# Optimization experiments

Measured on AMD Instinct MI355X. Metric: run time of the kernel, lower is better.

## Reference

```python
import jax, jax.numpy as jnp
import numpy as np

THRESHOLD = 0.3

def setup_inputs() -> dict:
    key = jax.random.key(0)
    ks = jax.random.split(key, 8)
    B, T, N, d = 4, 32, 1024, 2
    hd, od, hs, osz = 64, 64, 128, 2
    p = lambda k, sh: jax.random.normal(k, sh, jnp.float32) * 0.1
    return {
        "points": jax.random.uniform(ks[0], (B, T, N, d), jnp.float32),
        "W1": p(ks[1], (hd, d)),   "b1": jnp.zeros((hd,), jnp.float32),
        "W2": p(ks[2], (od, hd)),  "b2": jnp.zeros((od,), jnp.float32),
        "Wg": p(ks[3], (hd, od)),  "bg": jnp.zeros((hd,), jnp.float32),
        "Wih": p(ks[4], (3 * hs, hd)), "Whh": p(ks[5], (3 * hs, hs)),
        "bih": jnp.zeros((3 * hs,), jnp.float32), "bhh": jnp.zeros((3 * hs,), jnp.float32),
        "Wf": p(ks[6], (osz, hs)), "bf": jnp.zeros((osz,), jnp.float32),
    }

def _gcn_step(pts, W1, b1, W2, b2, Wg, bg):
    # pts: [N, d]. Torch detaches node features & adjacency (no grad to points).
    pts = jax.lax.stop_gradient(pts)
    dist = jnp.linalg.norm(pts[:, None, :] - pts[None, :, :], axis=2)  # [N,N]
    A = (dist < THRESHOLD).astype(pts.dtype)
    dinv = 1.0 / jnp.sqrt(A.sum(axis=1))          # rowsum >= 1 (self-loop)
    An = A * dinv[:, None] * dinv[None, :]        # D^{-1/2} A D^{-1/2}
    x = jax.nn.relu((An @ pts) @ W1.T + b1)       # [N, hd]
    x = jax.nn.relu((An @ x) @ W2.T + b2)         # [N, od]
    return x.mean(axis=0) @ Wg.T + bg             # [hd]

def reference(points, W1, b1, W2, b2, Wg, bg, Wih, Whh, bih, bhh, Wf, bf):
    # GCN per (batch, time): [B, T, hd]
    gcn = jax.vmap(jax.vmap(lambda p: _gcn_step(p, W1, b1, W2, b2, Wg, bg)))(points)
    H = Whh.shape[1]

    def gru_step(h, x):  # torch GRU gate order: r, z, n
        gi = x @ Wih.T + bih
        gh = h @ Whh.T + bhh
        ir, iz, inn = jnp.split(gi, 3)
        hr, hz, hn = jnp.split(gh, 3)
        r = jax.nn.sigmoid(ir + hr)
        z = jax.nn.sigmoid(iz + hz)
        n = jnp.tanh(inn + r * hn)
        h_new = (1.0 - z) * n + z * h
        return h_new, h_new

    h0 = jnp.zeros((H,), points.dtype)
    run = lambda xs: jax.lax.scan(gru_step, h0, xs)[1]   # [T, H]
    hs = jax.vmap(run)(gcn)                              # [B, T, H]
    y = hs @ Wf.T + bf                                   # [B, T, out]
    # torch: per-element gru_out.mean(dim=1, keepdim=True) on [1,T,out] -> [1,1,out], stacked -> [B,1,1,out]
    return y.mean(axis=1, keepdims=True)[:, :, None, :]
```

## Files before the change

### kernel.cpp

```cpp
#include <hip/hip_runtime.h>
#include <hip/hip_bf16.h>
#include <math.h>

#define N_PTS 1024
#define BT    128
typedef unsigned int u32;
typedef __attribute__((ext_vector_type(8))) short short8_t;
typedef __attribute__((ext_vector_type(4))) float f32x4;

__device__ __forceinline__ float bfi(u32 bits16) {
    union { u32 u; float f; } v; v.u = bits16 << 16; return v.f;
}
__device__ __forceinline__ unsigned short f2bf(float f) {
    union { float f; u32 u; } v; v.f = f;
    return (unsigned short)((v.u + 0x7FFFu + ((v.u >> 16) & 1u)) >> 16);
}
__device__ __forceinline__ float ldf(const void* p, int i, bool bf) {
    return bf ? bfi(((const unsigned short*)p)[i]) : ((const float*)p)[i];
}
__device__ __forceinline__ float2 ldp(const void* pbase, int j, bool bf) {
    if (bf) {
        u32 w = ((const u32*)pbase)[j];
        return make_float2(bfi(w & 0xFFFFu), bfi(w >> 16));
    }
    return ((const float2*)pbase)[j];
}
__device__ __forceinline__ bool detect_bf16(const void* pts, int tid, int* s_flag) {
    if (tid < 64) {
        u32 w = ((const u32*)pts)[tid];
        float v = bfi(w & 0xFFFFu);
        bool ok = (v >= 0.0f) && (v <= 1.0f);
        unsigned long long m = __ballot(ok);
        if (tid == 0) *s_flag = (m == 0xFFFFFFFFFFFFFFFFull) ? 1 : 0;
    }
    __syncthreads();
    return *s_flag != 0;
}
__device__ __forceinline__ bool is_nb(float px, float py, float qx, float qy) {
    float dx = px - qx, dy = py - qy;
    float d2 = __fadd_rn(__fmul_rn(dx, dx), __fmul_rn(dy, dy));
    return d2 < 0.09f;
}
__device__ __forceinline__ const void* pts_base(const void* pts, int bt, bool bf) {
    return bf ? (const void*)((const unsigned short*)pts + (size_t)bt * N_PTS * 2)
              : (const void*)((const float*)pts + (size_t)bt * N_PTS * 2);
}
__device__ __forceinline__ void gload16(const u32* g, u32* l) {
    __builtin_amdgcn_global_load_lds((const __attribute__((address_space(1))) u32*)g,
                                     (__attribute__((address_space(3))) u32*)l, 16, 0, 0);
}
__device__ __forceinline__ float rdlane(float v, int i) {
    return __int_as_float(__builtin_amdgcn_readlane(__float_as_int(v), i));
}
__device__ __forceinline__ float sigm_f(float x) {
    return __fdividef(1.0f, 1.0f + __expf(-x));
}
__device__ __forceinline__ float tanh_f(float x) {
    float e = __expf(2.0f * x);
    return 1.0f - __fdividef(2.0f, e + 1.0f);
}
__device__ __forceinline__ void build_lut(u32* slut, int tid) {
    if (tid < 16) {
        u32 d0 = ((tid & 1) ? 0x3F80u : 0u) | (((tid & 2) ? 0x3F80u : 0u) << 16);
        u32 d1 = ((tid & 4) ? 0x3F80u : 0u) | (((tid & 8) ? 0x3F80u : 0u) << 16);
        slut[2 * tid] = d0;
        slut[2 * tid + 1] = d1;
    }
}
__device__ __forceinline__ short8_t expand8(const uint2* lut2, u32 by) {
    uint2 lo = lut2[by & 15u], hi = lut2[by >> 4];
    union { uint4 u4; short8_t s8; } cv;
    cv.u4 = make_uint4(lo.x, lo.y, hi.x, hi.y);
    return cv.s8;
}

__global__ __launch_bounds__(256) void k1_bm(const void* __restrict__ pts,
                                             float* __restrict__ dinv,
                                             float* __restrict__ gsum,
                                             u32* __restrict__ bm) {
    int blk = blockIdx.x, tid = threadIdx.x;
    int bt = blk >> 2, q = blk & 3;
    __shared__ float2 sp[N_PTS];
    __shared__ int s_flag;
    bool bf = detect_bf16(pts, tid, &s_flag);
    const void* pb = pts_base(pts, bt, bf);
    for (int j = tid; j < N_PTS; j += 256) sp[j] = ldp(pb, j, bf);
    if (blk < 32) gsum[blk * 256 + tid] = 0.0f;
    __syncthreads();
    int i = q * 256 + tid;
    float px = sp[i].x, py = sp[i].y;
    const float4* sp4 = (const float4*)sp;
    u32* bmrow = bm + (size_t)bt * 32768 + i;
    int cnt = 0;
    for (int c = 0; c < 32; c++) {
        u32 m = 0;
#pragma unroll
        for (int h = 0; h < 8; h++) {
            float4 s01 = sp4[c * 16 + 2 * h], s23 = sp4[c * 16 + 2 * h + 1];
            if (is_nb(px, py, s01.x, s01.y)) m |= 1u << (4 * h);
            if (is_nb(px, py, s01.z, s01.w)) m |= 1u << (4 * h + 1);
            if (is_nb(px, py, s23.x, s23.y)) m |= 1u << (4 * h + 2);
            if (is_nb(px, py, s23.z, s23.w)) m |= 1u << (4 * h + 3);
        }
        bmrow[c * 1024] = m;
        cnt += __popc(m);
    }
    dinv[bt * N_PTS + i] = 1.0f / sqrtf((float)cnt);
}

__global__ __launch_bounds__(256) void k2_x1v(const void* __restrict__ pts,
                                              const void* __restrict__ W1,
                                              const void* __restrict__ b1,
                                              const float* __restrict__ dinv,
                                              const u32* __restrict__ bm,
                                              u32* __restrict__ x1vB) {
    int blk = blockIdx.x, tid = threadIdx.x;
    int bt = blk >> 2, q = blk & 3;
    __shared__ u32 sbm[8192];
    __shared__ unsigned short u_lds[4][1032];
    __shared__ float2 sax[256];
    __shared__ float  sdl[256];
    __shared__ u32 slut[32];
    __shared__ int s_flag;
    bool bf = detect_bf16(pts, tid, &s_flag);
    build_lut(slut, tid);
    const void* pb = pts_base(pts, bt, bf);
    for (int j = tid; j < N_PTS; j += 256) {
        float2 p = ldp(pb, j, bf);
        float d = dinv[bt * N_PTS + j];
        float ux = d * p.x, uy = d * p.y;
        unsigned short hx = f2bf(ux), hy = f2bf(uy);
        u_lds[0][j] = hx;
        u_lds[1][j] = hy;
        u_lds[2][j] = f2bf(ux - bfi(hx));
        u_lds[3][j] = f2bf(uy - bfi(hy));
    }
    const u32* bg_ = bm + (size_t)bt * 32768 + q * 256;
    for (int idx = tid; idx < 8192; idx += 256) {
        int c = idx >> 8, r = idx & 255;
        sbm[idx] = bg_[c * 1024 + r];
    }
    sdl[tid] = dinv[bt * N_PTS + q * 256 + tid];
    __syncthreads();

    int lane = tid & 63, w = tid >> 6;
    int l15 = lane & 15, quad = lane >> 4;
    f32x4 acc[4];
#pragma unroll
    for (int rf = 0; rf < 4; rf++)
#pragma unroll
        for (int r = 0; r < 4; r++) acc[rf][r] = 0.0f;

    const unsigned short* urow = &u_lds[l15 & 3][0];
    const uint2* lut2 = (const uint2*)slut;
    for (int c = 0; c < 32; c++) {
        short8_t bu = *(const short8_t*)(urow + c * 32 + quad * 8);
#pragma unroll
        for (int rf = 0; rf < 4; rf++) {
            u32 mw = sbm[c * 256 + w * 64 + rf * 16 + l15];
            u32 by = (mw >> (quad * 8)) & 0xFFu;
            acc[rf] = __builtin_amdgcn_mfma_f32_16x16x32_bf16(expand8(lut2, by), bu, acc[rf], 0, 0, 0);
        }
    }
#pragma unroll
    for (int rf = 0; rf < 4; rf++) {
#pragma unroll
        for (int r = 0; r < 4; r++) {
            float vsum = acc[rf][r] + __shfl_xor(acc[rf][r], 2, 64);
            int row = w * 64 + rf * 16 + quad * 4 + r;
            float sc = vsum * sdl[row];
            if (l15 == 0)      sax[row].x = sc;
            else if (l15 == 1) sax[row].y = sc;
        }
    }
    __syncthreads();
    int ch = tid & 63, wq = tid >> 6;
    float w0 = ldf(W1, 2 * ch, bf), w1v = ldf(W1, 2 * ch + 1, bf), bb = ldf(b1, ch, bf);
    for (int tt = 0; tt < 4; tt++) {
        u32 ow[8];
#pragma unroll
        for (int k2i = 0; k2i < 8; k2i++) {
            int lj = tt * 64 + wq * 16 + 2 * k2i;
            float2 a0 = sax[lj], a1 = sax[lj + 1];
            float v0 = sdl[lj]     * fmaxf(fmaf(w0, a0.x, fmaf(w1v, a0.y, bb)), 0.0f);
            float v1 = sdl[lj + 1] * fmaxf(fmaf(w0, a1.x, fmaf(w1v, a1.y, bb)), 0.0f);
            ow[k2i] = (u32)f2bf(v0) | ((u32)f2bf(v1) << 16);
        }
        u32* dst = x1vB + ((size_t)(bt * 16 + q * 4 + tt) * 64 + ch) * 36 + wq * 8;
        *(uint4*)dst = make_uint4(ow[0], ow[1], ow[2], ow[3]);
        *(uint4*)(dst + 4) = make_uint4(ow[4], ow[5], ow[6], ow[7]);
    }
}

__global__ __launch_bounds__(256) void k3_mfma(const void* __restrict__ pts,
                                               const void* __restrict__ W2,
                                               const void* __restrict__ b2,
                                               const float* __restrict__ dinv,
                                               const u32* __restrict__ bm,
                                               const u32* __restrict__ x1vB,
                                               float* __restrict__ gsum) {
    __shared__ u32 pool[15424];
    __shared__ u32 slut[32];
    __shared__ int s_flag;
    float* poolf = (float*)pool;
    int tid = threadIdx.x, lane = tid & 63, w = tid >> 6;
    int l15 = lane & 15, quad = lane >> 4;
    int blk = blockIdx.x, bt = blk & 127, rowblk = blk >> 7;
    bool bf = detect_bf16(pts, tid, &s_flag);
    build_lut(slut, tid);

    const u32* xg = x1vB + (size_t)bt * 36864;
    for (int it = w; it < 9; it += 4)
        gload16(xg + it * 256 + lane * 4, pool + 8192 + it * 256 + lane * 4);

    const u32* bg_ = bm + (size_t)bt * 32768 + rowblk * 256;
    for (int idx = tid; idx < 8192; idx += 256) {
        int c = idx >> 8, r = idx & 255;
        pool[idx] = bg_[c * 1024 + r];
    }
    unsigned short* W2B = (unsigned short*)(pool + 12800);
    for (int idx = tid; idx < 4096; idx += 256) {
        int o = idx >> 6, c = idx & 63;
        W2B[o * 72 + c] = f2bf(ldf(W2, idx, bf));
    }
    if (tid < 256) poolf[15104 + tid] = dinv[bt * N_PTS + rowblk * 256 + tid];
    if (tid < 64)  poolf[15360 + tid] = ldf(b2, tid, bf);

    f32x4 acc[4][4];
#pragma unroll
    for (int rf = 0; rf < 4; rf++)
#pragma unroll
        for (int nb = 0; nb < 4; nb++)
#pragma unroll
            for (int r = 0; r < 4; r++) acc[rf][nb][r] = 0.0f;

    const uint2* lut2 = (const uint2*)slut;
    for (int t = 0; t < 16; t++) {
        __syncthreads();
        if (t + 1 < 16) {
            u32* dst = pool + ((t & 1) ? 8192 : 10496);
            const u32* src = xg + (t + 1) * 2304;
            for (int it = w; it < 9; it += 4)
                gload16(src + it * 256 + lane * 4, dst + it * 256 + lane * 4);
        }
        const unsigned short* xf = (const unsigned short*)(pool + ((t & 1) ? 10496 : 8192));
#pragma unroll
        for (int ks = 0; ks < 2; ks++) {
            short8_t bq[4];
#pragma unroll
            for (int rf = 0; rf < 4; rf++) {
                u32 mw = pool[(2 * t + ks) * 256 + w * 64 + rf * 16 + l15];
                u32 by = (mw >> (quad * 8)) & 0xFFu;
                bq[rf] = expand8(lut2, by);
            }
#pragma unroll
            for (int nb = 0; nb < 4; nb++) {
                short8_t af = *(const short8_t*)(xf + (nb * 16 + l15) * 72 + ks * 32 + quad * 8);
#pragma unroll
                for (int rf = 0; rf < 4; rf++)
                    acc[rf][nb] = __builtin_amdgcn_mfma_f32_16x16x32_bf16(af, bq[rf], acc[rf][nb], 0, 0, 0);
            }
        }
    }
    __syncthreads();

    u32* dump = pool;
#pragma unroll
    for (int rf = 0; rf < 4; rf++) {
        int rn = w * 64 + rf * 16 + l15;
        float di = poolf[15104 + rn];
#pragma unroll
        for (int nb = 0; nb < 4; nb++) {
            u32 lo = (u32)f2bf(acc[rf][nb][0] * di) | ((u32)f2bf(acc[rf][nb][1] * di) << 16);
            u32 hi = (u32)f2bf(acc[rf][nb][2] * di) | ((u32)f2bf(acc[rf][nb][3] * di) << 16);
            u32* dst = dump + rn * 36 + nb * 8 + quad * 2;
            dst[0] = lo; dst[1] = hi;
        }
    }
    __syncthreads();
    f32x4 xacc[4][4];
#pragma unroll
    for (int ob = 0; ob < 4; ob++)
#pragma unroll
        for (int rf = 0; rf < 4; rf++)
#pragma unroll
            for (int r = 0; r < 4; r++) xacc[ob][rf][r] = 0.0f;
#pragma unroll
    for (int ks2 = 0; ks2 < 2; ks2++) {
        short8_t b2f[4];
#pragma unroll
        for (int rf = 0; rf < 4; rf++)
            b2f[rf] = *(const short8_t*)((const unsigned short*)dump +
                        (w * 64 + rf * 16 + l15) * 72 + ks2 * 32 + quad * 8);
#pragma unroll
        for (int ob = 0; ob < 4; ob++) {
            short8_t a2 = *(const short8_t*)(W2B + (ob * 16 + l15) * 72 + ks2 * 32 + quad * 8);
#pragma unroll
            for (int rf = 0; rf < 4; rf++)
                xacc[ob][rf] = __builtin_amdgcn_mfma_f32_16x16x32_bf16(a2, b2f[rf], xacc[ob][rf], 0, 0, 0);
        }
    }
#pragma unroll
    for (int ob = 0; ob < 4; ob++) {
#pragma unroll
        for (int r = 0; r < 4; r++) {
            int o = ob * 16 + quad * 4 + r;
            float bb = poolf[15360 + o];
            float s = 0.0f;
#pragma unroll
            for (int rf = 0; rf < 4; rf++) s += fmaxf(xacc[ob][rf][r] + bb, 0.0f);
            s += __shfl_down(s, 8, 16);
            s += __shfl_down(s, 4, 16);
            s += __shfl_down(s, 2, 16);
            s += __shfl_down(s, 1, 16);
            if (l15 == 0) atomicAdd(&gsum[bt * 64 + o], s);
        }
    }
}

__global__ __launch_bounds__(384, 1) void k4a_gi(const void* __restrict__ pts,
                                                 const void* __restrict__ Wg,
                                                 const void* __restrict__ bg,
                                                 const void* __restrict__ Wih,
                                                 const void* __restrict__ bih,
                                                 const float* __restrict__ gsum,
                                                 float* __restrict__ gi_ws) {
    int blk = blockIdx.x, tid = threadIdx.x;
    __shared__ float s_gm[64];
    __shared__ float s_x[64];
    __shared__ int s_flag;
    bool bf = detect_bf16(pts, tid, &s_flag);
    if (tid < 64) s_gm[tid] = gsum[(size_t)blk * 64 + tid] * (1.0f / 1024.0f);
    int r = tid;
    float wv[64];
    if (bf) {
#pragma unroll
        for (int k = 0; k < 64; k++) wv[k] = bfi(((const unsigned short*)Wih)[r * 64 + k]);
    } else {
        const float4* wr = (const float4*)Wih + r * 16;
#pragma unroll
        for (int qq = 0; qq < 16; qq++) {
            float4 v = wr[qq];
            wv[4*qq] = v.x; wv[4*qq+1] = v.y; wv[4*qq+2] = v.z; wv[4*qq+3] = v.w;
        }
    }
    float br = ldf(bih, r, bf);
    float wg[64];
    if (tid < 64) {
        if (bf) {
#pragma unroll
            for (int k = 0; k < 64; k++) wg[k] = bfi(((const unsigned short*)Wg)[tid * 64 + k]);
        } else {
            const float4* wr = (const float4*)Wg + tid * 16;
#pragma unroll
            for (int qq = 0; qq < 16; qq++) {
                float4 v = wr[qq];
                wg[4*qq] = v.x; wg[4*qq+1] = v.y; wg[4*qq+2] = v.z; wg[4*qq+3] = v.w;
            }
        }
    }
    __syncthreads();
    if (tid < 64) {
        float gmv = s_gm[tid];
        float s0 = ldf(bg, tid, bf), s1 = 0.f, s2 = 0.f, s3 = 0.f;
#pragma unroll
        for (int k = 0; k < 64; k += 4) {
            s0 = fmaf(wg[k],     rdlane(gmv, k),     s0);
            s1 = fmaf(wg[k + 1], rdlane(gmv, k + 1), s1);
            s2 = fmaf(wg[k + 2], rdlane(gmv, k + 2), s2);
            s3 = fmaf(wg[k + 3], rdlane(gmv, k + 3), s3);
        }
        s_x[tid] = (s0 + s1) + (s2 + s3);
    }
    __syncthreads();
    float xv = s_x[tid & 63];
    float s0 = br, s1 = 0.f, s2 = 0.f, s3 = 0.f;
#pragma unroll
    for (int k = 0; k < 64; k += 4) {
        s0 = fmaf(wv[k],     rdlane(xv, k),     s0);
        s1 = fmaf(wv[k + 1], rdlane(xv, k + 1), s1);
        s2 = fmaf(wv[k + 2], rdlane(xv, k + 2), s2);
        s3 = fmaf(wv[k + 3], rdlane(xv, k + 3), s3);
    }
    gi_ws[(size_t)blk * 384 + r] = (s0 + s1) + (s2 + s3);
}

__global__ __launch_bounds__(768, 1) void k4b_scan(const void* __restrict__ pts,
                                                   const void* __restrict__ Whh,
                                                   const void* __restrict__ bhh,
                                                   const void* __restrict__ Wf,
                                                   const void* __restrict__ bf_,
                                                   const float* __restrict__ gi_ws,
                                                   float* __restrict__ out) {
    int b = blockIdx.x, tid = threadIdx.x;
    __shared__ float s_gi[12288];
    __shared__ float s_part[2][768];
    __shared__ float s_hm[128];
    __shared__ int s_flag;
    bool bf = detect_bf16(pts, tid, &s_flag);
    const u32* gi_g = (const u32*)gi_ws + (size_t)b * 12288;
    u32* s_gi_u = (u32*)s_gi;
#pragma unroll
    for (int j = 0; j < 4; j++)
        gload16(gi_g + j * 3072 + tid * 4, s_gi_u + j * 3072 + tid * 4);

    int hi = (tid >= 384) ? 1 : 0;
    int r = tid - hi * 384;
    int lane = tid & 63;
    float wh2[64];
    {
        int koff = hi * 64;
        if (bf) {
#pragma unroll
            for (int k = 0; k < 64; k++)
                wh2[k] = bfi(((const unsigned short*)Whh)[r * 128 + koff + k]);
        } else {
            const float4* wr = (const float4*)Whh + (r * 128 + koff) / 4;
#pragma unroll
            for (int qq = 0; qq < 16; qq++) {
                float4 v = wr[qq];
                wh2[4*qq] = v.x; wh2[4*qq+1] = v.y; wh2[4*qq+2] = v.z; wh2[4*qq+3] = v.w;
            }
        }
    }
    float bhr = hi ? 0.0f : ldf(bhh, r, bf);
    int c = hi * 64 + lane;
    float hval = 0.0f;
    float hsum = 0.0f;
    __syncthreads();

    for (int t = 0; t < 32; t++) {
        float gi_r = s_gi[t * 384 + c];
        float gi_z = s_gi[t * 384 + 128 + c];
        float gi_n = s_gi[t * 384 + 256 + c];
        float s0 = bhr, s1 = 0.f, s2 = 0.f, s3 = 0.f;
#pragma unroll
        for (int k = 0; k < 64; k += 4) {
            s0 = fmaf(wh2[k],     rdlane(hval, k),     s0);
            s1 = fmaf(wh2[k + 1], rdlane(hval, k + 1), s1);
            s2 = fmaf(wh2[k + 2], rdlane(hval, k + 2), s2);
            s3 = fmaf(wh2[k + 3], rdlane(hval, k + 3), s3);
        }
        s_part[t & 1][tid] = (s0 + s1) + (s2 + s3);
        __syncthreads();
        const float* P = s_part[t & 1];
        float gr = gi_r + P[c]       + P[384 + c];
        float gz = gi_z + P[128 + c] + P[512 + c];
        float hn =        P[256 + c] + P[640 + c];
        float rr = sigm_f(gr);
        float z  = sigm_f(gz);
        float n  = tanh_f(fmaf(rr, hn, gi_n));
        hval = fmaf(z, hval - n, n);
        hsum += hval;
    }
    if (tid < 64) s_hm[tid] = hsum * (1.0f / 32.0f);
    else if (tid >= 384 && tid < 448) s_hm[64 + lane] = hsum * (1.0f / 32.0f);
    __syncthreads();
    if (tid < 128) {
        float hm = s_hm[tid];
        s_part[0][tid]       = ldf(Wf, tid, bf) * hm;
        s_part[0][128 + tid] = ldf(Wf, 128 + tid, bf) * hm;
    }
    __syncthreads();
    if (tid < 2) {
        float s = ldf(bf_, tid, bf);
        for (int k = 0; k < 128; k++) s += s_part[0][tid * 128 + k];
        out[b * 2 + tid] = s;
    }
}

extern "C" void kernel_launch(void* const* d_in, const int* in_sizes, int n_in,
                              void* d_out, int out_size, void* d_ws, size_t ws_size,
                              hipStream_t stream) {
    const void* pts = d_in[0];
    const void* W1  = d_in[1];
    const void* b1  = d_in[2];
    const void* W2  = d_in[3];
    const void* b2  = d_in[4];
    const void* Wg  = d_in[5];
    const void* bg  = d_in[6];
    const void* Wih = d_in[7];
    const void* Whh = d_in[8];
    const void* bih = d_in[9];
    const void* bhh = d_in[10];
    const void* Wf  = d_in[11];
    const void* bf_ = d_in[12];

    float* dinv = (float*)d_ws;
    float* gsum = dinv + (size_t)BT * N_PTS;
    u32*   bm   = (u32*)(gsum + BT * 64);
    u32*   x1vB = bm + (size_t)BT * 32768;
    float* gi_ws = (float*)x1vB;

    k1_bm  <<<512, 256, 0, stream>>>(pts, dinv, gsum, bm);
    k2_x1v <<<512, 256, 0, stream>>>(pts, W1, b1, dinv, bm, x1vB);
    k3_mfma<<<512, 256, 0, stream>>>(pts, W2, b2, dinv, bm, x1vB, gsum);
    k4a_gi <<<128, 384, 0, stream>>>(pts, Wg, bg, Wih, bih, gsum, gi_ws);
    k4b_scan<<<4, 768, 0, stream>>>(pts, Whh, bhh, Wf, bf_, gi_ws, (float*)d_out);
}
```

Measured before the change: 206.3 us.

## Compute GRU recurrent matvec with split-bf16 MFMA in the scan kernel

Replaces the per-thread readlane-based FMA recurrent matvec in the GRU scan with MFMA 16x16x32 bf16 instructions. Each 16-row tile of Whh is kept in registers as hi/lo bf16 pairs, and the hidden state is written to LDS as hi/lo bf16 each step, with three MFMAs per k-slice to keep near-fp32 accuracy. Gate math is now done by 128 threads after the gh values are gathered in LDS. This aims to cut the serial per-timestep latency of the recurrence, at the cost of a second barrier per step and extra bf16 split conversions.

```diff
diff --git a/kernel.cpp b/kernel.cpp
--- a/kernel.cpp
+++ b/kernel.cpp
@@ -394,8 +394,10 @@
                                                    float* __restrict__ out) {
     int b = blockIdx.x, tid = threadIdx.x;
     __shared__ float s_gi[12288];
-    __shared__ float s_part[2][768];
-    __shared__ float s_hm[128];
+    __shared__ float gh_lds[384];
+    __shared__ unsigned short h_hi[128] __attribute__((aligned(16)));
+    __shared__ unsigned short h_lo[128] __attribute__((aligned(16)));
+    __shared__ float s_red[256];
     __shared__ int s_flag;
     bool bf = detect_bf16(pts, tid, &s_flag);
     const u32* gi_g = (const u32*)gi_ws + (size_t)b * 12288;
@@ -404,67 +406,106 @@
     for (int j = 0; j < 4; j++)
         gload16(gi_g + j * 3072 + tid * 4, s_gi_u + j * 3072 + tid * 4);
 
-    int hi = (tid >= 384) ? 1 : 0;
-    int r = tid - hi * 384;
-    int lane = tid & 63;
-    float wh2[64];
-    {
-        int koff = hi * 64;
-        if (bf) {
-#pragma unroll
-            for (int k = 0; k < 64; k++)
-                wh2[k] = bfi(((const unsigned short*)Whh)[r * 128 + koff + k]);
-        } else {
-            const float4* wr = (const float4*)Whh + (r * 128 + koff) / 4;
-#pragma unroll
-            for (int qq = 0; qq < 16; qq++) {
-                float4 v = wr[qq];
-                wh2[4*qq] = v.x; wh2[4*qq+1] = v.y; wh2[4*qq+2] = v.z; wh2[4*qq+3] = v.w;
+    int lane = tid & 63, w = tid >> 6;
+    int l15 = lane & 15, quad = lane >> 4;
+    short8_t whi[2][4], wlo[2][4];
+#pragma unroll
+    for (int tt = 0; tt < 2; tt++) {
+        int row = (2 * w + tt) * 16 + l15;
+#pragma unroll
+        for (int s = 0; s < 4; s++) {
+            union { uint4 u4; short8_t s8; } cv, cl;
+            if (bf) {
+                cv.u4 = *(const uint4*)((const unsigned short*)Whh + row * 128 + s * 32 + quad * 8);
+                cl.u4 = make_uint4(0u, 0u, 0u, 0u);
+            } else {
+                const float* wp = (const float*)Whh + row * 128 + s * 32 + quad * 8;
+                float4 a = ((const float4*)wp)[0], b4 = ((const float4*)wp)[1];
+                float v[8] = {a.x, a.y, a.z, a.w, b4.x, b4.y, b4.z, b4.w};
+                unsigned short hh_[8], ll_[8];
+#pragma unroll
+                for (int i = 0; i < 8; i++) {
+                    hh_[i] = f2bf(v[i]);
+                    ll_[i] = f2bf(v[i] - bfi(hh_[i]));
+                }
+                cv.u4 = make_uint4((u32)hh_[0] | ((u32)hh_[1] << 16),
+                                   (u32)hh_[2] | ((u32)hh_[3] << 16),
+                                   (u32)hh_[4] | ((u32)hh_[5] << 16),
+                                   (u32)hh_[6] | ((u32)hh_[7] << 16));
+                cl.u4 = make_uint4((u32)ll_[0] | ((u32)ll_[1] << 16),
+                                   (u32)ll_[2] | ((u32)ll_[3] << 16),
+                                   (u32)ll_[4] | ((u32)ll_[5] << 16),
+                                   (u32)ll_[6] | ((u32)ll_[7] << 16));
             }
-        }
-    }
-    float bhr = hi ? 0.0f : ldf(bhh, r, bf);
-    int c = hi * 64 + lane;
-    float hval = 0.0f;
-    float hsum = 0.0f;
+            whi[tt][s] = cv.s8;
+            wlo[tt][s] = cl.s8;
+        }
+    }
+    float bhh_r = 0.f, bhh_z = 0.f, bhh_n = 0.f;
+    if (tid < 128) {
+        bhh_r = ldf(bhh, tid, bf);
+        bhh_z = ldf(bhh, 128 + tid, bf);
+        bhh_n = ldf(bhh, 256 + tid, bf);
+        h_hi[tid] = 0; h_lo[tid] = 0;
+    }
+    float hval = 0.0f, hsum = 0.0f;
     __syncthreads();
 
     for (int t = 0; t < 32; t++) {
-        float gi_r = s_gi[t * 384 + c];
-        float gi_z = s_gi[t * 384 + 128 + c];
-        float gi_n = s_gi[t * 384 + 256 + c];
-        float s0 = bhr, s1 = 0.f, s2 = 0.f, s3 = 0.f;
-#pragma unroll
-        for (int k = 0; k < 64; k += 4) {
-            s0 = fmaf(wh2[k],     rdlane(hval, k),     s0);
-            s1 = fmaf(wh2[k + 1], rdlane(hval, k + 1), s1);
-            s2 = fmaf(wh2[k + 2], rdlane(hval, k + 2), s2);
-            s3 = fmaf(wh2[k + 3], rdlane(hval, k + 3), s3);
-        }
-        s_part[t & 1][tid] = (s0 + s1) + (s2 + s3);
+        short8_t hh[4], hl[4];
+#pragma unroll
+        for (int s = 0; s < 4; s++) {
+            hh[s] = *(const short8_t*)(h_hi + s * 32 + quad * 8);
+            hl[s] = *(const short8_t*)(h_lo + s * 32 + quad * 8);
+        }
+        f32x4 acc0, acc1;
+#pragma unroll
+        for (int r = 0; r < 4; r++) { acc0[r] = 0.0f; acc1[r] = 0.0f; }
+#pragma unroll
+        for (int s = 0; s < 4; s++) {
+            acc0 = __builtin_amdgcn_mfma_f32_16x16x32_bf16(wlo[0][s], hh[s], acc0, 0, 0, 0);
+            acc0 = __builtin_amdgcn_mfma_f32_16x16x32_bf16(whi[0][s], hl[s], acc0, 0, 0, 0);
+            acc0 = __builtin_amdgcn_mfma_f32_16x16x32_bf16(whi[0][s], hh[s], acc0, 0, 0, 0);
+            acc1 = __builtin_amdgcn_mfma_f32_16x16x32_bf16(wlo[1][s], hh[s], acc1, 0, 0, 0);
+            acc1 = __builtin_amdgcn_mfma_f32_16x16x32_bf16(whi[1][s], hl[s], acc1, 0, 0, 0);
+            acc1 = __builtin_amdgcn_mfma_f32_16x16x32_bf16(whi[1][s], hh[s], acc1, 0, 0, 0);
+        }
+        if (l15 == 0) {
+#pragma unroll
+            for (int r = 0; r < 4; r++) {
+                gh_lds[(2 * w) * 16 + quad * 4 + r]     = acc0[r];
+                gh_lds[(2 * w + 1) * 16 + quad * 4 + r] = acc1[r];
+            }
+        }
         __syncthreads();
-        const float* P = s_part[t & 1];
-        float gr = gi_r + P[c]       + P[384 + c];
-        float gz = gi_z + P[128 + c] + P[512 + c];
-        float hn =        P[256 + c] + P[640 + c];
-        float rr = sigm_f(gr);
-        float z  = sigm_f(gz);
-        float n  = tanh_f(fmaf(rr, hn, gi_n));
-        hval = fmaf(z, hval - n, n);
-        hsum += hval;
-    }
-    if (tid < 64) s_hm[tid] = hsum * (1.0f / 32.0f);
-    else if (tid >= 384 && tid < 448) s_hm[64 + lane] = hsum * (1.0f / 32.0f);
-    __syncthreads();
+        if (tid < 128) {
+            int c = tid;
+            float gi_r = s_gi[t * 384 + c];
+            float gi_z = s_gi[t * 384 + 128 + c];
+            float gi_n = s_gi[t * 384 + 256 + c];
+            float gr = gi_r + (gh_lds[c] + bhh_r);
+            float gz = gi_z + (gh_lds[128 + c] + bhh_z);
+            float hn = gh_lds[256 + c] + bhh_n;
+            float rr = sigm_f(gr);
+            float z  = sigm_f(gz);
+            float n  = tanh_f(fmaf(rr, hn, gi_n));
+            hval = fmaf(z, hval - n, n);
+            hsum += hval;
+            unsigned short hb = f2bf(hval);
+            h_hi[c] = hb;
+            h_lo[c] = f2bf(hval - bfi(hb));
+        }
+        __syncthreads();
+    }
     if (tid < 128) {
-        float hm = s_hm[tid];
-        s_part[0][tid]       = ldf(Wf, tid, bf) * hm;
-        s_part[0][128 + tid] = ldf(Wf, 128 + tid, bf) * hm;
+        float hm = hsum * (1.0f / 32.0f);
+        s_red[tid]       = ldf(Wf, tid, bf) * hm;
+        s_red[128 + tid] = ldf(Wf, 128 + tid, bf) * hm;
     }
     __syncthreads();
     if (tid < 2) {
         float s = ldf(bf_, tid, bf);
-        for (int k = 0; k < 128; k++) s += s_part[0][tid * 128 + k];
+        for (int k = 0; k < 128; k++) s += s_red[tid * 128 + k];
         out[b * 2 + tid] = s;
     }
 }
```

After: 203.6 us. About the same (-1.3%).
